# Kernel optimization log

Measured on AMD Instinct MI355X. Metric: run time of the kernel, lower is better.

## Reference

```python
import jax, jax.numpy as jnp
import numpy as np

B = 128
T = 784
H = 256
N_CLASSES = 10


def setup_inputs() -> dict:
    key = jax.random.key(0)
    ks = jax.random.split(key, 7)
    s = 1.0 / np.sqrt(H)
    inputs = jax.random.normal(ks[0], (B, T), dtype=jnp.float32)
    # fixed permutation, matching np.random.RandomState(92916).permutation(784)
    perm = jnp.asarray(np.random.RandomState(92916).permutation(T), dtype=jnp.int32)
    W_ih = jax.random.uniform(ks[1], (4 * H, 1), jnp.float32, -s, s)
    W_hh = jax.random.uniform(ks[2], (4 * H, H), jnp.float32, -s, s)
    b_ih = jax.random.uniform(ks[3], (4 * H,), jnp.float32, -s, s)
    b_hh = jax.random.uniform(ks[4], (4 * H,), jnp.float32, -s, s)
    lin_W = jax.random.uniform(ks[5], (N_CLASSES, H), jnp.float32, -s, s)
    lin_b = jax.random.uniform(ks[6], (N_CLASSES,), jnp.float32, -s, s)
    return {"inputs": inputs, "perm": perm, "W_ih": W_ih, "W_hh": W_hh,
            "b_ih": b_ih, "b_hh": b_hh, "lin_W": lin_W, "lin_b": lin_b}


def reference(inputs, perm, W_ih, W_hh, b_ih, b_hh, lin_W, lin_b):
    # permuted sequential MNIST
    x = inputs[:, perm]                      # [B, T]
    b = b_ih + b_hh                          # [4H]
    w_in = W_ih[:, 0]                        # [4H], input size is 1

    def step(carry, x_t):
        h, c = carry                         # each [B, H]
        gates = x_t[:, None] * w_in[None, :] + h @ W_hh.T + b  # [B, 4H]
        i, f, g, o = jnp.split(gates, 4, axis=-1)
        i = jax.nn.sigmoid(i)
        f = jax.nn.sigmoid(f)
        g = jnp.tanh(g)
        o = jax.nn.sigmoid(o)
        c = f * c + i * g
        h = o * jnp.tanh(c)
        return (h, c), None

    h0 = jnp.zeros((x.shape[0], W_hh.shape[1]), dtype=x.dtype)
    (h, c), _ = jax.lax.scan(step, (h0, h0), x.T)  # scan over T, xs [T, B]
    return h @ lin_W.T + lin_b               # [B, n_classes]
```

## Files before the change

kernel.cpp:

```cpp
#include <hip/hip_runtime.h>

#define TSTEPS 784
#define BATCH  128
#define HID    256
#define WPG    8
#define BG     4
#define NGRP   (BATCH / BG)
#define COLS   32
#define RLOC   128
typedef unsigned long long u64;

__global__ void prep_x(const float* __restrict__ in, const int* __restrict__ perm,
                       float* __restrict__ xp) {
    int b = blockIdx.x;
    for (int t = threadIdx.x; t < TSTEPS; t += blockDim.x)
        xp[b * TSTEPS + t] = in[b * TSTEPS + perm[t]];
}

__global__ void prep_slots(u64* __restrict__ slots) {
    int i = blockIdx.x * blockDim.x + threadIdx.x;
    if (i < BATCH * HID)          slots[i] = 0ull;
    else if (i < 2 * BATCH * HID) slots[i] = 0xFFFFFFFF00000000ull;
}

__global__ __launch_bounds__(1024, 4) void lstm_kernel(
    const float* __restrict__ Whh, const float* __restrict__ Wih,
    const float* __restrict__ bih, const float* __restrict__ bhh,
    const float* __restrict__ xp, u64* __restrict__ slots)
{
    __shared__ float h_lds[BG * HID];
    __shared__ float gate_lds[BG * 132];
    __shared__ float x_lds[BG * TSTEPS];
    __shared__ float c_lds[BG * COLS];
    __shared__ float bias_lds[RLOC];
    __shared__ float win_lds[RLOC];

    const int tid = threadIdx.x;
    const int g       = blockIdx.x & 31;
    const int wgi     = blockIdx.x >> 5;
    const int B0      = g * BG;
    const int colbase = wgi * COLS;

    const int r = tid >> 3;
    const int s = tid & 7;
    const int gate = r >> 5;
    const int R = gate * 256 + colbase + (r & 31);

    float4 w0, w1, w2, w3, w4, w5, w6, w7;
    {
        const float4* wp = (const float4*)(Whh + R * HID + s * 32);
        w0 = wp[(0 + s) & 7]; w1 = wp[(1 + s) & 7];
        w2 = wp[(2 + s) & 7]; w3 = wp[(3 + s) & 7];
        w4 = wp[(4 + s) & 7]; w5 = wp[(5 + s) & 7];
        w6 = wp[(6 + s) & 7]; w7 = wp[(7 + s) & 7];
    }
    #define KEEP4(V) asm volatile("" : "+v"((V).x), "+v"((V).y), "+v"((V).z), "+v"((V).w))
    KEEP4(w0); KEEP4(w1); KEEP4(w2); KEEP4(w3);
    KEEP4(w4); KEEP4(w5); KEEP4(w6); KEEP4(w7);
    #undef KEEP4

    if (tid < RLOC) {
        int gr = (tid >> 5) * 256 + colbase + (tid & 31);
        bias_lds[tid] = bih[gr] + bhh[gr];
        win_lds[tid]  = Wih[gr];
    }
    #pragma unroll
    for (int b = 0; b < BG; ++b)
        if (tid < TSTEPS) x_lds[b * TSTEPS + tid] = xp[(B0 + b) * TSTEPS + tid];
    if (tid < BG * COLS) c_lds[tid] = 0.f;
    __syncthreads();

    const int pb = tid >> 8, pk = tid & 255;
    u64* const slot0 = slots + (B0 + pb) * HID + pk;
    u64* const slot1 = slots + BATCH * HID + (B0 + pb) * HID + pk;

    for (int t = 0; t < TSTEPS; ++t) {
        {
            u64* sp = (t & 1) ? slot1 : slot0;
            u64 v;
            do {
                v = __hip_atomic_load(sp, __ATOMIC_RELAXED, __HIP_MEMORY_SCOPE_AGENT);
            } while ((unsigned)(v >> 32) != (unsigned)t);
            h_lds[tid] = __uint_as_float((unsigned)v);
        }
        __syncthreads();

        float a0 = 0.f, a1 = 0.f, a2 = 0.f, a3 = 0.f;
        const float* hbase = h_lds + s * 32;
        #define DOT_STEP(d, wd)                                              \
        {                                                                    \
            int off = (((d) + s) & 7) * 4;                                   \
            float4 hq0 = *(const float4*)(hbase + off);                      \
            float4 hq1 = *(const float4*)(hbase + 256 + off);                \
            float4 hq2 = *(const float4*)(hbase + 512 + off);                \
            float4 hq3 = *(const float4*)(hbase + 768 + off);                \
            a0 = fmaf(wd.x, hq0.x, a0); a0 = fmaf(wd.y, hq0.y, a0);          \
            a0 = fmaf(wd.z, hq0.z, a0); a0 = fmaf(wd.w, hq0.w, a0);          \
            a1 = fmaf(wd.x, hq1.x, a1); a1 = fmaf(wd.y, hq1.y, a1);          \
            a1 = fmaf(wd.z, hq1.z, a1); a1 = fmaf(wd.w, hq1.w, a1);          \
            a2 = fmaf(wd.x, hq2.x, a2); a2 = fmaf(wd.y, hq2.y, a2);          \
            a2 = fmaf(wd.z, hq2.z, a2); a2 = fmaf(wd.w, hq2.w, a2);          \
            a3 = fmaf(wd.x, hq3.x, a3); a3 = fmaf(wd.y, hq3.y, a3);          \
            a3 = fmaf(wd.z, hq3.z, a3); a3 = fmaf(wd.w, hq3.w, a3);          \
        }
        DOT_STEP(0, w0) DOT_STEP(1, w1) DOT_STEP(2, w2) DOT_STEP(3, w3)
        DOT_STEP(4, w4) DOT_STEP(5, w5) DOT_STEP(6, w6) DOT_STEP(7, w7)
        #undef DOT_STEP

        #pragma unroll
        for (int m = 1; m < 8; m <<= 1) {
            a0 += __shfl_xor(a0, m, 64);
            a1 += __shfl_xor(a1, m, 64);
            a2 += __shfl_xor(a2, m, 64);
            a3 += __shfl_xor(a3, m, 64);
        }
        if (s < BG) {
            float sum = (s == 0) ? a0 : (s == 1) ? a1 : (s == 2) ? a2 : a3;
            float xv = x_lds[s * TSTEPS + t];
            float full = fmaf(win_lds[r], xv, sum + bias_lds[r]);
            float act;
            if (gate == 2) act = 2.f / (1.f + __expf(-2.f * full)) - 1.f;
            else           act = 1.f / (1.f + __expf(-full));
            gate_lds[s * 132 + r] = act;
        }
        __syncthreads();

        if (tid < BG * COLS) {
            int b = tid >> 5, j = tid & 31;
            float iv = gate_lds[b * 132 + j];
            float fv = gate_lds[b * 132 + 32 + j];
            float gv = gate_lds[b * 132 + 64 + j];
            float ov = gate_lds[b * 132 + 96 + j];
            float cn = fmaf(fv, c_lds[tid], iv * gv);
            c_lds[tid] = cn;
            float tc = 2.f / (1.f + __expf(-2.f * cn)) - 1.f;
            float hn = ov * tc;
            u64 val = ((u64)(unsigned)(t + 1) << 32) | (u64)__float_as_uint(hn);
            u64* dp = slots + ((t + 1) & 1) * (BATCH * HID)
                            + (B0 + b) * HID + colbase + j;
            __hip_atomic_store(dp, val, __ATOMIC_RELAXED, __HIP_MEMORY_SCOPE_AGENT);
        }
    }
}

__global__ void out_kernel(const u64* __restrict__ slots, const float* __restrict__ linW,
                           const float* __restrict__ linb, float* __restrict__ out) {
    __shared__ float hl[HID];
    int b = blockIdx.x;
    for (int k = threadIdx.x; k < HID; k += blockDim.x)
        hl[k] = __uint_as_float((unsigned)slots[b * HID + k]);
    __syncthreads();
    if (threadIdx.x < 10) {
        int n = threadIdx.x;
        float acc = linb[n];
        for (int k = 0; k < HID; ++k) acc = fmaf(hl[k], linW[n * HID + k], acc);
        out[b * 10 + n] = acc;
    }
}

extern "C" void kernel_launch(void* const* d_in, const int* in_sizes, int n_in,
                              void* d_out, int out_size, void* d_ws, size_t ws_size,
                              hipStream_t stream) {
    const float* inputs = (const float*)d_in[0];
    const int*   perm   = (const int*)d_in[1];
    const float* Wih    = (const float*)d_in[2];
    const float* Whh    = (const float*)d_in[3];
    const float* bih    = (const float*)d_in[4];
    const float* bhh    = (const float*)d_in[5];
    const float* linW   = (const float*)d_in[6];
    const float* linb   = (const float*)d_in[7];
    float* out = (float*)d_out;

    u64*   slots = (u64*)d_ws;
    float* xp    = (float*)(slots + 2 * BATCH * HID);

    prep_x<<<BATCH, 256, 0, stream>>>(inputs, perm, xp);
    prep_slots<<<(2 * BATCH * HID + 255) / 256, 256, 0, stream>>>(slots);
    lstm_kernel<<<NGRP * WPG, 1024, 0, stream>>>(Whh, Wih, bih, bhh, xp, slots);
    out_kernel<<<BATCH, 64, 0, stream>>>(slots, linW, linb, out);
}
```

Measured before the change: 2.244 ms.

## Remap LSTM recurrent matvec to 8 rows per wave with DPP/permlane reductions

```diff
diff --git a/kernel.cpp b/kernel.cpp
--- a/kernel.cpp
+++ b/kernel.cpp
@@ -7,7 +7,6 @@
 #define BG     4
 #define NGRP   (BATCH / BG)
 #define COLS   32
-#define RLOC   128
 typedef unsigned long long u64;
 
 __global__ void prep_x(const float* __restrict__ in, const int* __restrict__ perm,
@@ -23,47 +22,53 @@
     else if (i < 2 * BATCH * HID) slots[i] = 0xFFFFFFFF00000000ull;
 }
 
+#define DPP_ADD(x, ctl) asm("v_add_f32 %0, %1, %0 " ctl " row_mask:0xf bank_mask:0xf" \
+                            : "+v"(x) : "v"(x))
+
 __global__ __launch_bounds__(1024, 4) void lstm_kernel(
     const float* __restrict__ Whh, const float* __restrict__ Wih,
     const float* __restrict__ bih, const float* __restrict__ bhh,
     const float* __restrict__ xp, u64* __restrict__ slots)
 {
-    __shared__ float h_lds[BG * HID];
-    __shared__ float gate_lds[BG * 132];
+    __shared__ float h_lds[BG * 288];
+    __shared__ float gate_lds[4 * 132];
     __shared__ float x_lds[BG * TSTEPS];
     __shared__ float c_lds[BG * COLS];
-    __shared__ float bias_lds[RLOC];
-    __shared__ float win_lds[RLOC];
-
-    const int tid = threadIdx.x;
-    const int g       = blockIdx.x & 31;
-    const int wgi     = blockIdx.x >> 5;
-    const int B0      = g * BG;
+
+    const int tid  = threadIdx.x;
+    const int g    = blockIdx.x & 31;
+    const int wgi  = blockIdx.x >> 5;
+    const int B0   = g * BG;
     const int colbase = wgi * COLS;
 
-    const int r = tid >> 3;
-    const int s = tid & 7;
-    const int gate = r >> 5;
-    const int R = gate * 256 + colbase + (r & 31);
-
-    float4 w0, w1, w2, w3, w4, w5, w6, w7;
-    {
-        const float4* wp = (const float4*)(Whh + R * HID + s * 32);
-        w0 = wp[(0 + s) & 7]; w1 = wp[(1 + s) & 7];
-        w2 = wp[(2 + s) & 7]; w3 = wp[(3 + s) & 7];
-        w4 = wp[(4 + s) & 7]; w5 = wp[(5 + s) & 7];
-        w6 = wp[(6 + s) & 7]; w7 = wp[(7 + s) & 7];
+    const int wave = tid >> 6;
+    const int lane = tid & 63;
+    const int ks   = lane & 31;
+    const int b2   = lane >> 5;
+    const int gate = wave >> 2;
+    const int colw = (wave & 3) * 8;
+
+    float4 wA[8], wB[8];
+    #pragma unroll
+    for (int q = 0; q < 8; ++q) {
+        const float* wp = Whh + (gate * 256 + colbase + colw + q) * HID + 8 * ks;
+        wA[q] = *(const float4*)wp;
+        wB[q] = *(const float4*)(wp + 4);
     }
     #define KEEP4(V) asm volatile("" : "+v"((V).x), "+v"((V).y), "+v"((V).z), "+v"((V).w))
-    KEEP4(w0); KEEP4(w1); KEEP4(w2); KEEP4(w3);
-    KEEP4(w4); KEEP4(w5); KEEP4(w6); KEEP4(w7);
+    #pragma unroll
+    for (int q = 0; q < 8; ++q) { KEEP4(wA[q]); KEEP4(wB[q]); }
     #undef KEEP4
 
-    if (tid < RLOC) {
-        int gr = (tid >> 5) * 256 + colbase + (tid & 31);
-        bias_lds[tid] = bih[gr] + bhh[gr];
-        win_lds[tid]  = Wih[gr];
-    }
+    const int hl    = lane & 31;
+    const int widx  = hl & 7;
+    const int q_eff = (widx >> 1) + ((hl & 16) ? 4 : 0);
+    const int bsel  = 2 * b2 + (widx & 1);
+    const int rloc  = gate * 32 + colw + q_eff;
+    const int grow  = gate * 256 + colbase + colw + q_eff;
+    const float bias_r = bih[grow] + bhh[grow];
+    const float win_r  = Wih[grow];
+
     #pragma unroll
     for (int b = 0; b < BG; ++b)
         if (tid < TSTEPS) x_lds[b * TSTEPS + tid] = xp[(B0 + b) * TSTEPS + tid];
@@ -73,6 +78,7 @@
     const int pb = tid >> 8, pk = tid & 255;
     u64* const slot0 = slots + (B0 + pb) * HID + pk;
     u64* const slot1 = slots + BATCH * HID + (B0 + pb) * HID + pk;
+    const int hoff = pb * 288 + 9 * (pk >> 3) + (pk & 7);
 
     for (int t = 0; t < TSTEPS; ++t) {
         {
@@ -81,64 +87,96 @@
             do {
                 v = __hip_atomic_load(sp, __ATOMIC_RELAXED, __HIP_MEMORY_SCOPE_AGENT);
             } while ((unsigned)(v >> 32) != (unsigned)t);
-            h_lds[tid] = __uint_as_float((unsigned)v);
+            h_lds[hoff] = __uint_as_float((unsigned)v);
         }
         __syncthreads();
 
-        float a0 = 0.f, a1 = 0.f, a2 = 0.f, a3 = 0.f;
-        const float* hbase = h_lds + s * 32;
-        #define DOT_STEP(d, wd)                                              \
-        {                                                                    \
-            int off = (((d) + s) & 7) * 4;                                   \
-            float4 hq0 = *(const float4*)(hbase + off);                      \
-            float4 hq1 = *(const float4*)(hbase + 256 + off);                \
-            float4 hq2 = *(const float4*)(hbase + 512 + off);                \
-            float4 hq3 = *(const float4*)(hbase + 768 + off);                \
-            a0 = fmaf(wd.x, hq0.x, a0); a0 = fmaf(wd.y, hq0.y, a0);          \
-            a0 = fmaf(wd.z, hq0.z, a0); a0 = fmaf(wd.w, hq0.w, a0);          \
-            a1 = fmaf(wd.x, hq1.x, a1); a1 = fmaf(wd.y, hq1.y, a1);          \
-            a1 = fmaf(wd.z, hq1.z, a1); a1 = fmaf(wd.w, hq1.w, a1);          \
-            a2 = fmaf(wd.x, hq2.x, a2); a2 = fmaf(wd.y, hq2.y, a2);          \
-            a2 = fmaf(wd.z, hq2.z, a2); a2 = fmaf(wd.w, hq2.w, a2);          \
-            a3 = fmaf(wd.x, hq3.x, a3); a3 = fmaf(wd.y, hq3.y, a3);          \
-            a3 = fmaf(wd.z, hq3.z, a3); a3 = fmaf(wd.w, hq3.w, a3);          \
-        }
-        DOT_STEP(0, w0) DOT_STEP(1, w1) DOT_STEP(2, w2) DOT_STEP(3, w3)
-        DOT_STEP(4, w4) DOT_STEP(5, w5) DOT_STEP(6, w6) DOT_STEP(7, w7)
-        #undef DOT_STEP
-
-        #pragma unroll
-        for (int m = 1; m < 8; m <<= 1) {
-            a0 += __shfl_xor(a0, m, 64);
-            a1 += __shfl_xor(a1, m, 64);
-            a2 += __shfl_xor(a2, m, 64);
-            a3 += __shfl_xor(a3, m, 64);
-        }
-        if (s < BG) {
-            float sum = (s == 0) ? a0 : (s == 1) ? a1 : (s == 2) ? a2 : a3;
-            float xv = x_lds[s * TSTEPS + t];
-            float full = fmaf(win_lds[r], xv, sum + bias_lds[r]);
-            float act;
-            if (gate == 2) act = 2.f / (1.f + __expf(-2.f * full)) - 1.f;
-            else           act = 1.f / (1.f + __expf(-full));
-            gate_lds[s * 132 + r] = act;
-        }
+        float a[8][2];
+        const float* hb0 = h_lds + (2 * b2) * 288 + 9 * ks;
+        const float* hb1 = hb0 + 288;
+        {
+            float4 h00 = *(const float4*)(hb0);
+            float4 h01 = *(const float4*)(hb0 + 4);
+            #pragma unroll
+            for (int q = 0; q < 8; ++q) {
+                float s = wA[q].x * h00.x;
+                s = fmaf(wA[q].y, h00.y, s); s = fmaf(wA[q].z, h00.z, s);
+                s = fmaf(wA[q].w, h00.w, s); s = fmaf(wB[q].x, h01.x, s);
+                s = fmaf(wB[q].y, h01.y, s); s = fmaf(wB[q].z, h01.z, s);
+                s = fmaf(wB[q].w, h01.w, s);
+                a[q][0] = s;
+            }
+            float4 h10 = *(const float4*)(hb1);
+            float4 h11 = *(const float4*)(hb1 + 4);
+            #pragma unroll
+            for (int q = 0; q < 8; ++q) {
+                float s = wA[q].x * h10.x;
+                s = fmaf(wA[q].y, h10.y, s); s = fmaf(wA[q].z, h10.z, s);
+                s = fmaf(wA[q].w, h10.w, s); s = fmaf(wB[q].x, h11.x, s);
+                s = fmaf(wB[q].y, h11.y, s); s = fmaf(wB[q].z, h11.z, s);
+                s = fmaf(wB[q].w, h11.w, s);
+                a[q][1] = s;
+            }
+        }
+
+        #pragma unroll
+        for (int q = 0; q < 8; ++q) {
+            DPP_ADD(a[q][0], "quad_perm:[1,0,3,2]");
+            DPP_ADD(a[q][1], "quad_perm:[1,0,3,2]");
+        }
+        #pragma unroll
+        for (int q = 0; q < 8; ++q) {
+            DPP_ADD(a[q][0], "quad_perm:[2,3,0,1]");
+            DPP_ADD(a[q][1], "quad_perm:[2,3,0,1]");
+        }
+        #pragma unroll
+        for (int q = 0; q < 8; ++q) {
+            DPP_ADD(a[q][0], "row_ror:4");
+            DPP_ADD(a[q][1], "row_ror:4");
+        }
+        #pragma unroll
+        for (int q = 0; q < 8; ++q) {
+            DPP_ADD(a[q][0], "row_ror:8");
+            DPP_ADD(a[q][1], "row_ror:8");
+        }
+        float s00, s01, s10, s11, s20, s21, s30, s31;
+        #define TAIL(q, sq0, sq1) {                                           \
+            asm("v_permlane16_swap_b32 %0, %1" : "+v"(a[q][0]), "+v"(a[q+4][0])); \
+            sq0 = a[q][0] + a[q + 4][0];                                      \
+            asm("v_permlane16_swap_b32 %0, %1" : "+v"(a[q][1]), "+v"(a[q+4][1])); \
+            sq1 = a[q][1] + a[q + 4][1]; }
+        TAIL(0, s00, s01) TAIL(1, s10, s11) TAIL(2, s20, s21) TAIL(3, s30, s31)
+        #undef TAIL
+
+        float t0 = (widx & 1) ? s01 : s00;
+        float t1 = (widx & 1) ? s11 : s10;
+        float t2 = (widx & 1) ? s21 : s20;
+        float t3 = (widx & 1) ? s31 : s30;
+        float u0 = (widx & 2) ? t1 : t0;
+        float u1 = (widx & 2) ? t3 : t2;
+        float val = (widx & 4) ? u1 : u0;
+        float xv  = x_lds[bsel * TSTEPS + t];
+        val = fmaf(win_r, xv, val + bias_r);
+        float act = (gate == 2) ? (2.f / (1.f + __expf(-2.f * val)) - 1.f)
+                                : (1.f / (1.f + __expf(-val)));
+        if ((hl & 8) == 0)
+            gate_lds[gate * 132 + bsel * 33 + colw + q_eff] = act;
         __syncthreads();
 
         if (tid < BG * COLS) {
-            int b = tid >> 5, j = tid & 31;
-            float iv = gate_lds[b * 132 + j];
-            float fv = gate_lds[b * 132 + 32 + j];
-            float gv = gate_lds[b * 132 + 64 + j];
-            float ov = gate_lds[b * 132 + 96 + j];
+            int b = tid >> 5, col = tid & 31;
+            float iv = gate_lds[0 * 132 + b * 33 + col];
+            float fv = gate_lds[1 * 132 + b * 33 + col];
+            float gv = gate_lds[2 * 132 + b * 33 + col];
+            float ov = gate_lds[3 * 132 + b * 33 + col];
             float cn = fmaf(fv, c_lds[tid], iv * gv);
             c_lds[tid] = cn;
             float tc = 2.f / (1.f + __expf(-2.f * cn)) - 1.f;
             float hn = ov * tc;
-            u64 val = ((u64)(unsigned)(t + 1) << 32) | (u64)__float_as_uint(hn);
+            u64 valw = ((u64)(unsigned)(t + 1) << 32) | (u64)__float_as_uint(hn);
             u64* dp = slots + ((t + 1) & 1) * (BATCH * HID)
-                            + (B0 + b) * HID + colbase + j;
-            __hip_atomic_store(dp, val, __ATOMIC_RELAXED, __HIP_MEMORY_SCOPE_AGENT);
+                            + (B0 + b) * HID + colbase + col;
+            __hip_atomic_store(dp, valw, __ATOMIC_RELAXED, __HIP_MEMORY_SCOPE_AGENT);
         }
     }
 }
```

After: 2.570 ms. 1.15x slower.

## Interleave gate rows per column, fuse cell update via shuffles, use packed FMA

Applied to the files above, without the earlier changes.

```diff
diff --git a/kernel.cpp b/kernel.cpp
--- a/kernel.cpp
+++ b/kernel.cpp
@@ -9,6 +9,8 @@
 #define COLS   32
 #define RLOC   128
 typedef unsigned long long u64;
+typedef float v4f __attribute__((ext_vector_type(4)));
+typedef float v2f __attribute__((ext_vector_type(2)));
 
 __global__ void prep_x(const float* __restrict__ in, const int* __restrict__ perm,
                        float* __restrict__ xp) {
@@ -22,6 +24,9 @@
     if (i < BATCH * HID)          slots[i] = 0ull;
     else if (i < 2 * BATCH * HID) slots[i] = 0xFFFFFFFF00000000ull;
 }
+
+#define PK_FMA(acc, a, b) \
+    asm("v_pk_fma_f32 %0, %1, %2, %0" : "+v"(acc) : "v"(a), "v"(b))
 
 __global__ __launch_bounds__(1024, 4) void lstm_kernel(
     const float* __restrict__ Whh, const float* __restrict__ Wih,
@@ -29,7 +34,6 @@
     const float* __restrict__ xp, u64* __restrict__ slots)
 {
     __shared__ float h_lds[BG * HID];
-    __shared__ float gate_lds[BG * 132];
     __shared__ float x_lds[BG * TSTEPS];
     __shared__ float c_lds[BG * COLS];
     __shared__ float bias_lds[RLOC];
@@ -41,26 +45,28 @@
     const int B0      = g * BG;
     const int colbase = wgi * COLS;
 
-    const int r = tid >> 3;
-    const int s = tid & 7;
-    const int gate = r >> 5;
-    const int R = gate * 256 + colbase + (r & 31);
-
-    float4 w0, w1, w2, w3, w4, w5, w6, w7;
+    const int r    = tid >> 3;
+    const int s    = tid & 7;
+    const int lane = tid & 63;
+    const int col  = r >> 2;
+    const int gate = r & 3;
+    const int R = gate * 256 + colbase + col;
+
+    v4f w0, w1, w2, w3, w4, w5, w6, w7;
     {
-        const float4* wp = (const float4*)(Whh + R * HID + s * 32);
+        const v4f* wp = (const v4f*)(Whh + R * HID + s * 32);
         w0 = wp[(0 + s) & 7]; w1 = wp[(1 + s) & 7];
         w2 = wp[(2 + s) & 7]; w3 = wp[(3 + s) & 7];
         w4 = wp[(4 + s) & 7]; w5 = wp[(5 + s) & 7];
         w6 = wp[(6 + s) & 7]; w7 = wp[(7 + s) & 7];
     }
-    #define KEEP4(V) asm volatile("" : "+v"((V).x), "+v"((V).y), "+v"((V).z), "+v"((V).w))
-    KEEP4(w0); KEEP4(w1); KEEP4(w2); KEEP4(w3);
-    KEEP4(w4); KEEP4(w5); KEEP4(w6); KEEP4(w7);
-    #undef KEEP4
+    #define KEEPV(V) asm volatile("" : "+v"(V))
+    KEEPV(w0); KEEPV(w1); KEEPV(w2); KEEPV(w3);
+    KEEPV(w4); KEEPV(w5); KEEPV(w6); KEEPV(w7);
+    #undef KEEPV
 
     if (tid < RLOC) {
-        int gr = (tid >> 5) * 256 + colbase + (tid & 31);
+        int gr = (tid & 3) * 256 + colbase + (tid >> 2);
         bias_lds[tid] = bih[gr] + bhh[gr];
         win_lds[tid]  = Wih[gr];
     }
@@ -74,38 +80,54 @@
     u64* const slot0 = slots + (B0 + pb) * HID + pk;
     u64* const slot1 = slots + BATCH * HID + (B0 + pb) * HID + pk;
 
+    const bool is_upd = ((lane >> 3) & 3) == 0 && s < BG;
+
     for (int t = 0; t < TSTEPS; ++t) {
         {
             u64* sp = (t & 1) ? slot1 : slot0;
-            u64 v;
-            do {
-                v = __hip_atomic_load(sp, __ATOMIC_RELAXED, __HIP_MEMORY_SCOPE_AGENT);
-            } while ((unsigned)(v >> 32) != (unsigned)t);
-            h_lds[tid] = __uint_as_float((unsigned)v);
+            u64 p0 = __hip_atomic_load(sp, __ATOMIC_RELAXED, __HIP_MEMORY_SCOPE_AGENT);
+            u64 p1 = __hip_atomic_load(sp, __ATOMIC_RELAXED, __HIP_MEMORY_SCOPE_AGENT);
+            while ((unsigned)(p0 >> 32) != (unsigned)t) {
+                p0 = p1;
+                p1 = __hip_atomic_load(sp, __ATOMIC_RELAXED, __HIP_MEMORY_SCOPE_AGENT);
+            }
+            h_lds[tid] = __uint_as_float((unsigned)p0);
         }
         __syncthreads();
 
-        float a0 = 0.f, a1 = 0.f, a2 = 0.f, a3 = 0.f;
+        v2f acc0 = {0.f, 0.f}, acc1 = {0.f, 0.f}, acc2 = {0.f, 0.f}, acc3 = {0.f, 0.f};
         const float* hbase = h_lds + s * 32;
-        #define DOT_STEP(d, wd)                                              \
-        {                                                                    \
-            int off = (((d) + s) & 7) * 4;                                   \
-            float4 hq0 = *(const float4*)(hbase + off);                      \
-            float4 hq1 = *(const float4*)(hbase + 256 + off);                \
-            float4 hq2 = *(const float4*)(hbase + 512 + off);                \
-            float4 hq3 = *(const float4*)(hbase + 768 + off);                \
-            a0 = fmaf(wd.x, hq0.x, a0); a0 = fmaf(wd.y, hq0.y, a0);          \
-            a0 = fmaf(wd.z, hq0.z, a0); a0 = fmaf(wd.w, hq0.w, a0);          \
-            a1 = fmaf(wd.x, hq1.x, a1); a1 = fmaf(wd.y, hq1.y, a1);          \
-            a1 = fmaf(wd.z, hq1.z, a1); a1 = fmaf(wd.w, hq1.w, a1);          \
-            a2 = fmaf(wd.x, hq2.x, a2); a2 = fmaf(wd.y, hq2.y, a2);          \
-            a2 = fmaf(wd.z, hq2.z, a2); a2 = fmaf(wd.w, hq2.w, a2);          \
-            a3 = fmaf(wd.x, hq3.x, a3); a3 = fmaf(wd.y, hq3.y, a3);          \
-            a3 = fmaf(wd.z, hq3.z, a3); a3 = fmaf(wd.w, hq3.w, a3);          \
+        #define DOT_STEP(d, wd)                                               \
+        {                                                                     \
+            int off = (((d) + s) & 7) * 4;                                    \
+            v4f hq0 = *(const v4f*)(hbase + off);                             \
+            v4f hq1 = *(const v4f*)(hbase + 256 + off);                       \
+            v4f hq2 = *(const v4f*)(hbase + 512 + off);                       \
+            v4f hq3 = *(const v4f*)(hbase + 768 + off);                       \
+            v2f wlo = __builtin_shufflevector(wd, wd, 0, 1);                  \
+            v2f whi = __builtin_shufflevector(wd, wd, 2, 3);                  \
+            v2f hl, hh;                                                       \
+            hl = __builtin_shufflevector(hq0, hq0, 0, 1);                     \
+            hh = __builtin_shufflevector(hq0, hq0, 2, 3);                     \
+            PK_FMA(acc0, wlo, hl); PK_FMA(acc0, whi, hh);                     \
+            hl = __builtin_shufflevector(hq1, hq1, 0, 1);                     \
+            hh = __builtin_shufflevector(hq1, hq1, 2, 3);                     \
+            PK_FMA(acc1, wlo, hl); PK_FMA(acc1, whi, hh);                     \
+            hl = __builtin_shufflevector(hq2, hq2, 0, 1);                     \
+            hh = __builtin_shufflevector(hq2, hq2, 2, 3);                     \
+            PK_FMA(acc2, wlo, hl); PK_FMA(acc2, whi, hh);                     \
+            hl = __builtin_shufflevector(hq3, hq3, 0, 1);                     \
+            hh = __builtin_shufflevector(hq3, hq3, 2, 3);                     \
+            PK_FMA(acc3, wlo, hl); PK_FMA(acc3, whi, hh);                     \
         }
         DOT_STEP(0, w0) DOT_STEP(1, w1) DOT_STEP(2, w2) DOT_STEP(3, w3)
         DOT_STEP(4, w4) DOT_STEP(5, w5) DOT_STEP(6, w6) DOT_STEP(7, w7)
         #undef DOT_STEP
+
+        float a0 = acc0.x + acc0.y;
+        float a1 = acc1.x + acc1.y;
+        float a2 = acc2.x + acc2.y;
+        float a3 = acc3.x + acc3.y;
 
         #pragma unroll
         for (int m = 1; m < 8; m <<= 1) {
@@ -114,32 +136,32 @@
             a2 += __shfl_xor(a2, m, 64);
             a3 += __shfl_xor(a3, m, 64);
         }
-        if (s < BG) {
-            float sum = (s == 0) ? a0 : (s == 1) ? a1 : (s == 2) ? a2 : a3;
-            float xv = x_lds[s * TSTEPS + t];
-            float full = fmaf(win_lds[r], xv, sum + bias_lds[r]);
-            float act;
-            if (gate == 2) act = 2.f / (1.f + __expf(-2.f * full)) - 1.f;
-            else           act = 1.f / (1.f + __expf(-full));
-            gate_lds[s * 132 + r] = act;
-        }
-        __syncthreads();
-
-        if (tid < BG * COLS) {
-            int b = tid >> 5, j = tid & 31;
-            float iv = gate_lds[b * 132 + j];
-            float fv = gate_lds[b * 132 + 32 + j];
-            float gv = gate_lds[b * 132 + 64 + j];
-            float ov = gate_lds[b * 132 + 96 + j];
-            float cn = fmaf(fv, c_lds[tid], iv * gv);
-            c_lds[tid] = cn;
+
+        float sum = (s == 0) ? a0 : (s == 1) ? a1 : (s == 2) ? a2 : a3;
+        float xv  = x_lds[s * TSTEPS + t];
+        float full = fmaf(win_lds[r], xv, sum + bias_lds[r]);
+        float pre = (gate == 2) ? 2.f * full : full;
+        float e   = __expf(-pre);
+        float rec = 1.f / (1.f + e);
+        float act = (gate == 2) ? fmaf(2.f, rec, -1.f) : rec;
+
+        float act_f = __shfl_down(act, 8, 64);
+        float act_g = __shfl_down(act, 16, 64);
+        float act_o = __shfl_down(act, 24, 64);
+
+        if (is_upd) {
+            int b = s;
+            int ci = col * 4 + b;
+            float cn = fmaf(act_f, c_lds[ci], act * act_g);
             float tc = 2.f / (1.f + __expf(-2.f * cn)) - 1.f;
-            float hn = ov * tc;
+            float hn = act_o * tc;
             u64 val = ((u64)(unsigned)(t + 1) << 32) | (u64)__float_as_uint(hn);
             u64* dp = slots + ((t + 1) & 1) * (BATCH * HID)
-                            + (B0 + b) * HID + colbase + j;
+                            + (B0 + b) * HID + colbase + col;
             __hip_atomic_store(dp, val, __ATOMIC_RELAXED, __HIP_MEMORY_SCOPE_AGENT);
-        }
+            c_lds[ci] = cn;
+        }
+        __syncthreads();
     }
 }
 
```

After: 3.138 ms. 1.4x slower.

## Interleave two batch groups per workgroup and use packed FP32 FMA

Applied to the files above, without the earlier changes.

```diff
diff --git a/kernel.cpp b/kernel.cpp
--- a/kernel.cpp
+++ b/kernel.cpp
@@ -5,10 +5,12 @@
 #define HID    256
 #define WPG    8
 #define BG     4
-#define NGRP   (BATCH / BG)
+#define NSET   16
 #define COLS   32
 #define RLOC   128
 typedef unsigned long long u64;
+typedef float v4f __attribute__((ext_vector_type(4)));
+typedef float v2f __attribute__((ext_vector_type(2)));
 
 __global__ void prep_x(const float* __restrict__ in, const int* __restrict__ perm,
                        float* __restrict__ xp) {
@@ -23,22 +25,28 @@
     else if (i < 2 * BATCH * HID) slots[i] = 0xFFFFFFFF00000000ull;
 }
 
+#define PK_FMA(acc, a, b) \
+    asm("v_pk_fma_f32 %0, %1, %2, %0" : "+v"(acc) : "v"(a), "v"(b))
+
 __global__ __launch_bounds__(1024, 4) void lstm_kernel(
     const float* __restrict__ Whh, const float* __restrict__ Wih,
     const float* __restrict__ bih, const float* __restrict__ bhh,
     const float* __restrict__ xp, u64* __restrict__ slots)
 {
-    __shared__ float h_lds[BG * HID];
+    __shared__ float h_A[BG * HID];
+    __shared__ float h_B[BG * HID];
     __shared__ float gate_lds[BG * 132];
-    __shared__ float x_lds[BG * TSTEPS];
-    __shared__ float c_lds[BG * COLS];
+    __shared__ float x_lds[2 * BG * TSTEPS];
+    __shared__ float c_A[BG * COLS];
+    __shared__ float c_B[BG * COLS];
     __shared__ float bias_lds[RLOC];
     __shared__ float win_lds[RLOC];
 
     const int tid = threadIdx.x;
-    const int g       = blockIdx.x & 31;
-    const int wgi     = blockIdx.x >> 5;
-    const int B0      = g * BG;
+    const int set     = blockIdx.x & 15;
+    const int wgi     = blockIdx.x >> 4;
+    const int B0A     = set * 8;
+    const int B0B     = set * 8 + 4;
     const int colbase = wgi * COLS;
 
     const int r = tid >> 3;
@@ -46,18 +54,14 @@
     const int gate = r >> 5;
     const int R = gate * 256 + colbase + (r & 31);
 
-    float4 w0, w1, w2, w3, w4, w5, w6, w7;
+    v4f w0, w1, w2, w3, w4, w5, w6, w7;
     {
-        const float4* wp = (const float4*)(Whh + R * HID + s * 32);
+        const v4f* wp = (const v4f*)(Whh + R * HID + s * 32);
         w0 = wp[(0 + s) & 7]; w1 = wp[(1 + s) & 7];
         w2 = wp[(2 + s) & 7]; w3 = wp[(3 + s) & 7];
         w4 = wp[(4 + s) & 7]; w5 = wp[(5 + s) & 7];
         w6 = wp[(6 + s) & 7]; w7 = wp[(7 + s) & 7];
     }
-    #define KEEP4(V) asm volatile("" : "+v"((V).x), "+v"((V).y), "+v"((V).z), "+v"((V).w))
-    KEEP4(w0); KEEP4(w1); KEEP4(w2); KEEP4(w3);
-    KEEP4(w4); KEEP4(w5); KEEP4(w6); KEEP4(w7);
-    #undef KEEP4
 
     if (tid < RLOC) {
         int gr = (tid >> 5) * 256 + colbase + (tid & 31);
@@ -65,82 +69,136 @@
         win_lds[tid]  = Wih[gr];
     }
     #pragma unroll
-    for (int b = 0; b < BG; ++b)
-        if (tid < TSTEPS) x_lds[b * TSTEPS + tid] = xp[(B0 + b) * TSTEPS + tid];
-    if (tid < BG * COLS) c_lds[tid] = 0.f;
+    for (int b = 0; b < 2 * BG; ++b)
+        if (tid < TSTEPS) x_lds[b * TSTEPS + tid] = xp[(B0A + b) * TSTEPS + tid];
+    if (tid < BG * COLS) { c_A[tid] = 0.f; c_B[tid] = 0.f; }
     __syncthreads();
 
     const int pb = tid >> 8, pk = tid & 255;
-    u64* const slot0 = slots + (B0 + pb) * HID + pk;
-    u64* const slot1 = slots + BATCH * HID + (B0 + pb) * HID + pk;
+    u64* const slotA0 = slots + (B0A + pb) * HID + pk;
+    u64* const slotA1 = slots + BATCH * HID + (B0A + pb) * HID + pk;
+    u64* const slotB0 = slots + (B0B + pb) * HID + pk;
+    u64* const slotB1 = slots + BATCH * HID + (B0B + pb) * HID + pk;
+
+    #define DO_DOT(HSRC)                                                      \
+        v2f acc0 = {0.f, 0.f}, acc1 = {0.f, 0.f},                             \
+            acc2 = {0.f, 0.f}, acc3 = {0.f, 0.f};                             \
+        {                                                                     \
+            const float* hbase = (HSRC) + s * 32;                             \
+            DOT_STEP(0, w0) DOT_STEP(1, w1) DOT_STEP(2, w2) DOT_STEP(3, w3)   \
+            DOT_STEP(4, w4) DOT_STEP(5, w5) DOT_STEP(6, w6) DOT_STEP(7, w7)   \
+        }                                                                     \
+        float a0 = acc0.x + acc0.y;                                           \
+        float a1 = acc1.x + acc1.y;                                           \
+        float a2 = acc2.x + acc2.y;                                           \
+        float a3 = acc3.x + acc3.y;                                           \
+        _Pragma("unroll")                                                     \
+        for (int m = 1; m < 8; m <<= 1) {                                     \
+            a0 += __shfl_xor(a0, m, 64);                                      \
+            a1 += __shfl_xor(a1, m, 64);                                      \
+            a2 += __shfl_xor(a2, m, 64);                                      \
+            a3 += __shfl_xor(a3, m, 64);                                      \
+        }
+
+    #define DOT_STEP(d, wd)                                                   \
+    {                                                                         \
+        int off = (((d) + s) & 7) * 4;                                        \
+        v4f hq0 = *(const v4f*)(hbase + off);                                 \
+        v4f hq1 = *(const v4f*)(hbase + 256 + off);                           \
+        v4f hq2 = *(const v4f*)(hbase + 512 + off);                           \
+        v4f hq3 = *(const v4f*)(hbase + 768 + off);                           \
+        v2f wlo = __builtin_shufflevector(wd, wd, 0, 1);                      \
+        v2f whi = __builtin_shufflevector(wd, wd, 2, 3);                      \
+        PK_FMA(acc0, wlo, __builtin_shufflevector(hq0, hq0, 0, 1));           \
+        PK_FMA(acc0, whi, __builtin_shufflevector(hq0, hq0, 2, 3));           \
+        PK_FMA(acc1, wlo, __builtin_shufflevector(hq1, hq1, 0, 1));           \
+        PK_FMA(acc1, whi, __builtin_shufflevector(hq1, hq1, 2, 3));           \
+        PK_FMA(acc2, wlo, __builtin_shufflevector(hq2, hq2, 0, 1));           \
+        PK_FMA(acc2, whi, __builtin_shufflevector(hq2, hq2, 2, 3));           \
+        PK_FMA(acc3, wlo, __builtin_shufflevector(hq3, hq3, 0, 1));           \
+        PK_FMA(acc3, whi, __builtin_shufflevector(hq3, hq3, 2, 3));           \
+    }
 
     for (int t = 0; t < TSTEPS; ++t) {
-        {
-            u64* sp = (t & 1) ? slot1 : slot0;
+        asm volatile("" : "+v"(w0), "+v"(w1), "+v"(w2), "+v"(w3),
+                          "+v"(w4), "+v"(w5), "+v"(w6), "+v"(w7));
+
+        {
+            u64* sp = (t & 1) ? slotA1 : slotA0;
             u64 v;
-            do {
-                v = __hip_atomic_load(sp, __ATOMIC_RELAXED, __HIP_MEMORY_SCOPE_AGENT);
+            do { v = __hip_atomic_load(sp, __ATOMIC_RELAXED, __HIP_MEMORY_SCOPE_AGENT);
             } while ((unsigned)(v >> 32) != (unsigned)t);
-            h_lds[tid] = __uint_as_float((unsigned)v);
-        }
-        __syncthreads();
-
-        float a0 = 0.f, a1 = 0.f, a2 = 0.f, a3 = 0.f;
-        const float* hbase = h_lds + s * 32;
-        #define DOT_STEP(d, wd)                                              \
-        {                                                                    \
-            int off = (((d) + s) & 7) * 4;                                   \
-            float4 hq0 = *(const float4*)(hbase + off);                      \
-            float4 hq1 = *(const float4*)(hbase + 256 + off);                \
-            float4 hq2 = *(const float4*)(hbase + 512 + off);                \
-            float4 hq3 = *(const float4*)(hbase + 768 + off);                \
-            a0 = fmaf(wd.x, hq0.x, a0); a0 = fmaf(wd.y, hq0.y, a0);          \
-            a0 = fmaf(wd.z, hq0.z, a0); a0 = fmaf(wd.w, hq0.w, a0);          \
-            a1 = fmaf(wd.x, hq1.x, a1); a1 = fmaf(wd.y, hq1.y, a1);          \
-            a1 = fmaf(wd.z, hq1.z, a1); a1 = fmaf(wd.w, hq1.w, a1);          \
-            a2 = fmaf(wd.x, hq2.x, a2); a2 = fmaf(wd.y, hq2.y, a2);          \
-            a2 = fmaf(wd.z, hq2.z, a2); a2 = fmaf(wd.w, hq2.w, a2);          \
-            a3 = fmaf(wd.x, hq3.x, a3); a3 = fmaf(wd.y, hq3.y, a3);          \
-            a3 = fmaf(wd.z, hq3.z, a3); a3 = fmaf(wd.w, hq3.w, a3);          \
-        }
-        DOT_STEP(0, w0) DOT_STEP(1, w1) DOT_STEP(2, w2) DOT_STEP(3, w3)
-        DOT_STEP(4, w4) DOT_STEP(5, w5) DOT_STEP(6, w6) DOT_STEP(7, w7)
-        #undef DOT_STEP
-
-        #pragma unroll
-        for (int m = 1; m < 8; m <<= 1) {
-            a0 += __shfl_xor(a0, m, 64);
-            a1 += __shfl_xor(a1, m, 64);
-            a2 += __shfl_xor(a2, m, 64);
-            a3 += __shfl_xor(a3, m, 64);
-        }
-        if (s < BG) {
-            float sum = (s == 0) ? a0 : (s == 1) ? a1 : (s == 2) ? a2 : a3;
-            float xv = x_lds[s * TSTEPS + t];
-            float full = fmaf(win_lds[r], xv, sum + bias_lds[r]);
-            float act;
-            if (gate == 2) act = 2.f / (1.f + __expf(-2.f * full)) - 1.f;
-            else           act = 1.f / (1.f + __expf(-full));
-            gate_lds[s * 132 + r] = act;
-        }
-        __syncthreads();
-
+            h_A[tid] = __uint_as_float((unsigned)v);
+        }
+        __syncthreads();
+        {
+            DO_DOT(h_A)
+            if (s < BG) {
+                float sum = (s == 0) ? a0 : (s == 1) ? a1 : (s == 2) ? a2 : a3;
+                float xv = x_lds[s * TSTEPS + t];
+                float full = fmaf(win_lds[r], xv, sum + bias_lds[r]);
+                float pre = (gate == 2) ? 2.f * full : full;
+                float rec = 1.f / (1.f + __expf(-pre));
+                float act = (gate == 2) ? fmaf(2.f, rec, -1.f) : rec;
+                gate_lds[s * 132 + r] = act;
+            }
+        }
+        __syncthreads();
         if (tid < BG * COLS) {
             int b = tid >> 5, j = tid & 31;
             float iv = gate_lds[b * 132 + j];
             float fv = gate_lds[b * 132 + 32 + j];
             float gv = gate_lds[b * 132 + 64 + j];
             float ov = gate_lds[b * 132 + 96 + j];
-            float cn = fmaf(fv, c_lds[tid], iv * gv);
-            c_lds[tid] = cn;
+            float cn = fmaf(fv, c_A[tid], iv * gv);
+            c_A[tid] = cn;
             float tc = 2.f / (1.f + __expf(-2.f * cn)) - 1.f;
             float hn = ov * tc;
             u64 val = ((u64)(unsigned)(t + 1) << 32) | (u64)__float_as_uint(hn);
             u64* dp = slots + ((t + 1) & 1) * (BATCH * HID)
-                            + (B0 + b) * HID + colbase + j;
+                            + (B0A + b) * HID + colbase + j;
             __hip_atomic_store(dp, val, __ATOMIC_RELAXED, __HIP_MEMORY_SCOPE_AGENT);
         }
-    }
+
+        {
+            u64* sp = (t & 1) ? slotB1 : slotB0;
+            u64 v;
+            do { v = __hip_atomic_load(sp, __ATOMIC_RELAXED, __HIP_MEMORY_SCOPE_AGENT);
+            } while ((unsigned)(v >> 32) != (unsigned)t);
+            h_B[tid] = __uint_as_float((unsigned)v);
+        }
+        __syncthreads();
+        {
+            DO_DOT(h_B)
+            if (s < BG) {
+                float sum = (s == 0) ? a0 : (s == 1) ? a1 : (s == 2) ? a2 : a3;
+                float xv = x_lds[(BG + s) * TSTEPS + t];
+                float full = fmaf(win_lds[r], xv, sum + bias_lds[r]);
+                float pre = (gate == 2) ? 2.f * full : full;
+                float rec = 1.f / (1.f + __expf(-pre));
+                float act = (gate == 2) ? fmaf(2.f, rec, -1.f) : rec;
+                gate_lds[s * 132 + r] = act;
+            }
+        }
+        __syncthreads();
+        if (tid < BG * COLS) {
+            int b = tid >> 5, j = tid & 31;
+            float iv = gate_lds[b * 132 + j];
+            float fv = gate_lds[b * 132 + 32 + j];
+            float gv = gate_lds[b * 132 + 64 + j];
+            float ov = gate_lds[b * 132 + 96 + j];
+            float cn = fmaf(fv, c_B[tid], iv * gv);
+            c_B[tid] = cn;
+            float tc = 2.f / (1.f + __expf(-2.f * cn)) - 1.f;
+            float hn = ov * tc;
+            u64 val = ((u64)(unsigned)(t + 1) << 32) | (u64)__float_as_uint(hn);
+            u64* dp = slots + ((t + 1) & 1) * (BATCH * HID)
+                            + (B0B + b) * HID + colbase + j;
+            __hip_atomic_store(dp, val, __ATOMIC_RELAXED, __HIP_MEMORY_SCOPE_AGENT);
+        }
+    }
+    #undef DOT_STEP
+    #undef DO_DOT
 }
 
 __global__ void out_kernel(const u64* __restrict__ slots, const float* __restrict__ linW,
@@ -176,6 +234,6 @@
 
     prep_x<<<BATCH, 256, 0, stream>>>(inputs, perm, xp);
     prep_slots<<<(2 * BATCH * HID + 255) / 256, 256, 0, stream>>>(slots);
-    lstm_kernel<<<NGRP * WPG, 1024, 0, stream>>>(Whh, Wih, bih, bhh, xp, slots);
+    lstm_kernel<<<NSET * WPG, 1024, 0, stream>>>(Whh, Wih, bih, bhh, xp, slots);
     out_kernel<<<BATCH, 64, 0, stream>>>(slots, linW, linb, out);
 }
```

After: 3.593 ms. 1.6x slower.
